# Performance work log

Measured on AMD Instinct MI355X. Metric: run time of the kernel, lower is better.

Reference implementation:

```python
import jax, jax.numpy as jnp
import numpy as np

N = 500_000      # number of gaussians
F = 32           # grid feature dim (WavePlaneField.feat_dim)
R = 128          # plane resolution
W = 256          # MLP width
BOUNDS = 1.6     # scene aabb half-extent (args.bounds)


def setup_inputs() -> dict:
    key = jax.random.key(0)
    ks = jax.random.split(key, 16)
    s = lambda d: 1.0 / np.sqrt(d)
    return {
        "rays_pts_emb": jax.random.normal(ks[0], (N, 3), jnp.float32),
        "rotations_emb": jax.random.normal(ks[1], (N, 4), jnp.float32),
        "scale_emb": jax.random.uniform(ks[2], (N, 3), jnp.float32),
        "shs_emb": jax.random.normal(ks[3], (N, 16, 3), jnp.float32),
        "view_dir": jax.random.normal(ks[4], (N, 3), jnp.float32),
        "time_emb": jax.random.uniform(ks[5], (N, 1), jnp.float32),
        "h_emb": jax.random.normal(ks[6], (N, 2), jnp.float32),
        # multiplicative k-planes: init near 1 so products are well-scaled
        "space_planes": 1.0 + 0.1 * jax.random.normal(ks[7], (3, R, R, F), jnp.float32),
        "time_planes": 1.0 + 0.1 * jax.random.normal(ks[8], (3, R, R, F), jnp.float32),
        "w_enc": s(F) * jax.random.normal(ks[9], (F, W), jnp.float32),
        "b_enc": jnp.zeros((W,), jnp.float32),
        "w1": s(W) * jax.random.normal(ks[10], (W, W), jnp.float32),
        "b1": jnp.zeros((W,), jnp.float32),
        "w2": s(W) * jax.random.normal(ks[11], (W, 16 * 3), jnp.float32),
        "b2": jnp.zeros((16 * 3,), jnp.float32),
    }


def _interp2d(plane, u, v):
    """Bilinear sample plane [R,R,F] at normalized coords u,v in [0,1]. -> [N,F]"""
    Rr = plane.shape[0]
    x = jnp.clip(u, 0.0, 1.0) * (Rr - 1)
    y = jnp.clip(v, 0.0, 1.0) * (Rr - 1)
    x0 = jnp.clip(jnp.floor(x), 0, Rr - 2).astype(jnp.int32)
    y0 = jnp.clip(jnp.floor(y), 0, Rr - 2).astype(jnp.int32)
    fx = (x - x0)[:, None]
    fy = (y - y0)[:, None]
    p00 = plane[y0, x0]
    p01 = plane[y0, x0 + 1]
    p10 = plane[y0 + 1, x0]
    p11 = plane[y0 + 1, x0 + 1]
    return (p00 * (1 - fx) + p01 * fx) * (1 - fy) + (p10 * (1 - fx) + p11 * fx) * fy


def _covariance(scale, rotation):
    """3DGS: L = R(q) @ diag(s); cov = L L^T; return 6 unique entries [N,6]."""
    q = rotation / jnp.linalg.norm(rotation, axis=-1, keepdims=True)
    r, x, y, z = q[:, 0], q[:, 1], q[:, 2], q[:, 3]
    Rm = jnp.stack([
        jnp.stack([1 - 2 * (y * y + z * z), 2 * (x * y - r * z), 2 * (x * z + r * y)], -1),
        jnp.stack([2 * (x * y + r * z), 1 - 2 * (x * x + z * z), 2 * (y * z - r * x)], -1),
        jnp.stack([2 * (x * z - r * y), 2 * (y * z + r * x), 1 - 2 * (x * x + y * y)], -1),
    ], axis=1)  # [N,3,3]
    L = Rm * scale[:, None, :]                      # R @ diag(s)
    cov = jnp.einsum('nij,nkj->nik', L, L)          # L @ L^T
    return jnp.stack([cov[:, 0, 0], cov[:, 0, 1], cov[:, 0, 2],
                      cov[:, 1, 1], cov[:, 1, 2], cov[:, 2, 2]], axis=-1)


def reference(rays_pts_emb, rotations_emb, scale_emb, shs_emb, view_dir, time_emb,
              h_emb, space_planes, time_planes, w_enc, b_enc, w1, b1, w2, b2):
    # quaternion -> covariance (passed into grid in original; grid lookup itself
    # only needs positions/time, so symm is computed but unused downstream)
    symm = _covariance(scale_emb, rotations_emb)

    pts = rays_pts_emb[:, :3]
    pn = jnp.clip(pts / BOUNDS, -1.0, 1.0) * 0.5 + 0.5  # aabb-normalize to [0,1]
    xn, yn, zn = pn[:, 0], pn[:, 1], pn[:, 2]
    t = jnp.clip(time_emb[:, 0], 0.0, 1.0)

    space = (_interp2d(space_planes[0], xn, yn)
             * _interp2d(space_planes[1], xn, zn)
             * _interp2d(space_planes[2], yn, zn))          # [N,F]
    spacetime = (_interp2d(time_planes[0], xn, t)
                 * _interp2d(time_planes[1], yn, t)
                 * _interp2d(time_planes[2], zn, t))        # [N,F]

    feat = (space * spacetime) @ w_enc + b_enc              # spacetime_enc (Linear only)
    h = jax.nn.relu(feat) @ w1 + b1                         # shs_deform MLP
    d = jax.nn.relu(h) @ w2 + b2                            # [N,48]
    shs = shs_emb + d.reshape(-1, 16, 3)

    del symm  # original forward discards covariance after grid query
    return (rays_pts_emb, rotations_emb, h_emb[:, 0:1], shs)
```

## Files before the change

kernel.cpp:

```cpp
#include <hip/hip_runtime.h>
#include <hip/hip_fp16.h>

#define NPTS 500000
#define RPLANE 128
#define FDIM 32
#define PLSZ (RPLANE * RPLANE * FDIM)

typedef __bf16 bfx8 __attribute__((ext_vector_type(8)));
typedef float f32x4 __attribute__((ext_vector_type(4)));

__device__ __forceinline__ unsigned short f2bf(float f) {
    unsigned int u = __builtin_bit_cast(unsigned int, f);
    unsigned int r = (u + 0x7FFFu + ((u >> 16) & 1u)) >> 16;
    return (unsigned short)r;
}

__device__ __forceinline__ bfx8 ld_frag_g(const unsigned short* p) {
    uint4 raw = *(const uint4*)p;
    return __builtin_bit_cast(bfx8, raw);
}

struct h4v { __half2 a, b; };

__device__ __forceinline__ float4 interp4h(const __half* __restrict__ plane,
                                           float u, float v, int f0) {
    float x = fminf(fmaxf(u, 0.f), 1.f) * 127.0f;
    float y = fminf(fmaxf(v, 0.f), 1.f) * 127.0f;
    float xf = fminf(fmaxf(floorf(x), 0.f), 126.f);
    float yf = fminf(fmaxf(floorf(y), 0.f), 126.f);
    int x0 = (int)xf, y0 = (int)yf;
    float fx = x - xf, fy = y - yf;
    const __half* p = plane + (size_t)(y0 * RPLANE + x0) * FDIM + f0;
    h4v c00 = *(const h4v*)p;
    h4v c01 = *(const h4v*)(p + FDIM);
    h4v c10 = *(const h4v*)(p + RPLANE * FDIM);
    h4v c11 = *(const h4v*)(p + RPLANE * FDIM + FDIM);
    float2 a00l = __half22float2(c00.a), a00h = __half22float2(c00.b);
    float2 a01l = __half22float2(c01.a), a01h = __half22float2(c01.b);
    float2 a10l = __half22float2(c10.a), a10h = __half22float2(c10.b);
    float2 a11l = __half22float2(c11.a), a11h = __half22float2(c11.b);
    float w00 = (1.f - fx) * (1.f - fy);
    float w01 = fx * (1.f - fy);
    float w10 = (1.f - fx) * fy;
    float w11 = fx * fy;
    float4 r;
    r.x = a00l.x * w00 + a01l.x * w01 + a10l.x * w10 + a11l.x * w11;
    r.y = a00l.y * w00 + a01l.y * w01 + a10l.y * w10 + a11l.y * w11;
    r.z = a00h.x * w00 + a01h.x * w01 + a10h.x * w10 + a11h.x * w11;
    r.w = a00h.y * w00 + a01h.y * w01 + a10h.y * w10 + a11h.y * w11;
    return r;
}

__global__ void prep_all(const float* __restrict__ wenc, const float* __restrict__ w1,
                         const float* __restrict__ w2, const float* __restrict__ spf,
                         const float* __restrict__ tpf,
                         unsigned short* __restrict__ wf, __half* __restrict__ ph) {
    const int WTOT = 86016;
    const int PTOT = 6 * PLSZ;
    const int total = WTOT + PTOT;
    for (int i = blockIdx.x * blockDim.x + threadIdx.x; i < total;
         i += gridDim.x * blockDim.x) {
        if (i < WTOT) {
            const float* W;
            unsigned short* dst;
            int K, Ncols, idx;
            if (i < 8192)       { W = wenc; K = 32;  Ncols = 256; idx = i;         dst = wf; }
            else if (i < 73728) { W = w1;   K = 256; Ncols = 256; idx = i - 8192;  dst = wf + 8192; }
            else                { W = w2;   K = 256; Ncols = 48;  idx = i - 73728; dst = wf + 73728; }
            int j = idx & 7;
            int l = (idx >> 3) & 63;
            int b = idx >> 9;
            int KS = K >> 5;
            int ct = b / KS;
            int ks = b - ct * KS;
            int k = ks * 32 + ((l >> 4) << 3) + j;
            int col = ct * 16 + (l & 15);
            dst[idx] = f2bf(W[(size_t)k * Ncols + col]);
        } else {
            int j = i - WTOT;
            float v = (j < 3 * PLSZ) ? spf[j] : tpf[j - 3 * PLSZ];
            ph[j] = __float2half(v);
        }
    }
}

__global__ void pass_copy(const float* __restrict__ rays, const float* __restrict__ rot,
                          const float* __restrict__ h, float* __restrict__ out) {
    const int total = NPTS * 8;
    for (int i = blockIdx.x * blockDim.x + threadIdx.x; i < total; i += gridDim.x * blockDim.x) {
        float v;
        if (i < NPTS * 3) v = rays[i];
        else if (i < NPTS * 7) v = rot[i - NPTS * 3];
        else v = h[(i - NPTS * 7) * 2];
        out[i] = v;
    }
}

__global__ __launch_bounds__(256, 2) void fused2(
    const float* __restrict__ rays, const float* __restrict__ tme,
    const float* __restrict__ shs,
    const __half* __restrict__ sp, const __half* __restrict__ tp,
    const unsigned short* __restrict__ wf,
    const float* __restrict__ benc, const float* __restrict__ b1v,
    const float* __restrict__ b2v, float* __restrict__ out) {
    __shared__ unsigned short feat[4][32][40];
    __shared__ unsigned short hbuf[4][32][264];
    const int tid = threadIdx.x;
    const int wid = tid >> 6;
    const int lane = tid & 63;
    const int p0 = blockIdx.x * 128 + wid * 32;
    if (p0 >= NPTS) return;
    unsigned short(*fw)[40] = feat[wid];
    unsigned short(*hw)[264] = hbuf[wid];

#pragma unroll
    for (int it = 0; it < 4; ++it) {
        int task = it * 64 + lane;
        int pl = task >> 3;
        int fg = task & 7;
        int p = p0 + pl;
        float4 g = make_float4(0.f, 0.f, 0.f, 0.f);
        if (p < NPTS) {
            float px = rays[p * 3 + 0], py = rays[p * 3 + 1], pz = rays[p * 3 + 2];
            const float inv = 0.625f;
            float xn = fminf(fmaxf(px * inv, -1.f), 1.f) * 0.5f + 0.5f;
            float yn = fminf(fmaxf(py * inv, -1.f), 1.f) * 0.5f + 0.5f;
            float zn = fminf(fmaxf(pz * inv, -1.f), 1.f) * 0.5f + 0.5f;
            float t = fminf(fmaxf(tme[p], 0.f), 1.f);
            int f0 = fg << 2;
            float4 s0 = interp4h(sp, xn, yn, f0);
            float4 s1 = interp4h(sp + PLSZ, xn, zn, f0);
            float4 s2 = interp4h(sp + 2 * PLSZ, yn, zn, f0);
            float4 t0 = interp4h(tp, xn, t, f0);
            float4 t1 = interp4h(tp + PLSZ, yn, t, f0);
            float4 t2 = interp4h(tp + 2 * PLSZ, zn, t, f0);
            g.x = s0.x * s1.x * s2.x * t0.x * t1.x * t2.x;
            g.y = s0.y * s1.y * s2.y * t0.y * t1.y * t2.y;
            g.z = s0.z * s1.z * s2.z * t0.z * t1.z * t2.z;
            g.w = s0.w * s1.w * s2.w * t0.w * t1.w * t2.w;
        }
        ushort4 gb;
        gb.x = f2bf(g.x); gb.y = f2bf(g.y); gb.z = f2bf(g.z); gb.w = f2bf(g.w);
        *(ushort4*)&fw[pl][fg << 2] = gb;
    }

    const int lrow = lane & 15;
    const int lk8 = (lane >> 4) << 3;
    const int drow = (lane >> 4) << 2;

    bfx8 a0 = __builtin_bit_cast(bfx8, *(const uint4*)&fw[lrow][lk8]);
    bfx8 a1 = __builtin_bit_cast(bfx8, *(const uint4*)&fw[16 + lrow][lk8]);
#pragma unroll
    for (int ct = 0; ct < 16; ++ct) {
        bfx8 b = ld_frag_g(wf + (size_t)ct * 512 + lane * 8);
        f32x4 z = {0.f, 0.f, 0.f, 0.f};
        f32x4 d0 = __builtin_amdgcn_mfma_f32_16x16x32_bf16(a0, b, z, 0, 0, 0);
        f32x4 d1 = __builtin_amdgcn_mfma_f32_16x16x32_bf16(a1, b, z, 0, 0, 0);
        float bias = benc[ct * 16 + lrow];
#pragma unroll
        for (int r = 0; r < 4; ++r) {
            hw[drow + r][ct * 16 + lrow] = f2bf(fmaxf(d0[r] + bias, 0.f));
            hw[16 + drow + r][ct * 16 + lrow] = f2bf(fmaxf(d1[r] + bias, 0.f));
        }
    }

    const unsigned short* w1f = wf + 8192;
    bfx8 A0[8], A1[8];
#pragma unroll
    for (int ks = 0; ks < 8; ++ks) {
        A0[ks] = __builtin_bit_cast(bfx8, *(const uint4*)&hw[lrow][ks * 32 + lk8]);
        A1[ks] = __builtin_bit_cast(bfx8, *(const uint4*)&hw[16 + lrow][ks * 32 + lk8]);
    }
#pragma unroll
    for (int ct = 0; ct < 16; ++ct) {
        f32x4 acc0 = {0.f, 0.f, 0.f, 0.f};
        f32x4 acc1 = {0.f, 0.f, 0.f, 0.f};
#pragma unroll
        for (int ks = 0; ks < 8; ++ks) {
            bfx8 B = ld_frag_g(w1f + (size_t)(ct * 8 + ks) * 512 + lane * 8);
            acc0 = __builtin_amdgcn_mfma_f32_16x16x32_bf16(A0[ks], B, acc0, 0, 0, 0);
            acc1 = __builtin_amdgcn_mfma_f32_16x16x32_bf16(A1[ks], B, acc1, 0, 0, 0);
        }
        float bias = b1v[ct * 16 + lrow];
#pragma unroll
        for (int r = 0; r < 4; ++r) {
            hw[drow + r][ct * 16 + lrow] = f2bf(fmaxf(acc0[r] + bias, 0.f));
            hw[16 + drow + r][ct * 16 + lrow] = f2bf(fmaxf(acc1[r] + bias, 0.f));
        }
    }

    const unsigned short* w2f = wf + 73728;
    bfx8 C0[8], C1[8];
#pragma unroll
    for (int ks = 0; ks < 8; ++ks) {
        C0[ks] = __builtin_bit_cast(bfx8, *(const uint4*)&hw[lrow][ks * 32 + lk8]);
        C1[ks] = __builtin_bit_cast(bfx8, *(const uint4*)&hw[16 + lrow][ks * 32 + lk8]);
    }
#pragma unroll
    for (int ct = 0; ct < 3; ++ct) {
        f32x4 acc0 = {0.f, 0.f, 0.f, 0.f};
        f32x4 acc1 = {0.f, 0.f, 0.f, 0.f};
#pragma unroll
        for (int ks = 0; ks < 8; ++ks) {
            bfx8 B = ld_frag_g(w2f + (size_t)(ct * 8 + ks) * 512 + lane * 8);
            acc0 = __builtin_amdgcn_mfma_f32_16x16x32_bf16(C0[ks], B, acc0, 0, 0, 0);
            acc1 = __builtin_amdgcn_mfma_f32_16x16x32_bf16(C1[ks], B, acc1, 0, 0, 0);
        }
        int col = ct * 16 + lrow;
        float bias = b2v[col];
#pragma unroll
        for (int r = 0; r < 4; ++r) {
            int pr = p0 + drow + r;
            if (pr < NPTS)
                out[(size_t)NPTS * 8 + (size_t)pr * 48 + col] =
                    shs[(size_t)pr * 48 + col] + acc0[r] + bias;
            int pr2 = p0 + 16 + drow + r;
            if (pr2 < NPTS)
                out[(size_t)NPTS * 8 + (size_t)pr2 * 48 + col] =
                    shs[(size_t)pr2 * 48 + col] + acc1[r] + bias;
        }
    }
}

extern "C" void kernel_launch(void* const* d_in, const int* in_sizes, int n_in,
                              void* d_out, int out_size, void* d_ws, size_t ws_size,
                              hipStream_t stream) {
    const float* rays = (const float*)d_in[0];
    const float* rot  = (const float*)d_in[1];
    const float* shs  = (const float*)d_in[3];
    const float* tme  = (const float*)d_in[5];
    const float* h_e  = (const float*)d_in[6];
    const float* spf  = (const float*)d_in[7];
    const float* tpf  = (const float*)d_in[8];
    const float* wenc = (const float*)d_in[9];
    const float* benc = (const float*)d_in[10];
    const float* w1   = (const float*)d_in[11];
    const float* b1v  = (const float*)d_in[12];
    const float* w2   = (const float*)d_in[13];
    const float* b2v  = (const float*)d_in[14];
    float* out = (float*)d_out;
    unsigned short* wf = (unsigned short*)d_ws;
    __half* ph = (__half*)(wf + 86016);

    prep_all<<<3408, 256, 0, stream>>>(wenc, w1, w2, spf, tpf, wf, ph);
    pass_copy<<<2048, 256, 0, stream>>>(rays, rot, h_e, out);
    fused2<<<(NPTS + 127) / 128, 256, 0, stream>>>(
        rays, tme, shs, ph, ph + 3 * PLSZ, wf, benc, b1v, b2v, out);
}
```

Before: 239.1 us.

## Shrink per-wave tile to 16 points, compute features in MFMA layout with half2 math

Each wave now handles 16 points instead of 32, and the fused kernel's launch bounds allow 4 blocks per CU, so occupancy should rise. Each lane computes 8 features for one point directly in the MFMA A-fragment layout. That removes the feature staging buffer in shared memory and uses 16-byte plane loads. Bilinear interpolation and the product of the six planes are done in packed fp16 arithmetic, which cuts ALU work but lowers precision. The hidden activations are stored in a smaller XOR-swizzled shared buffer to avoid bank conflicts, at the cost of reloading the weight fragments for only half as many points per load.

```diff
diff --git a/kernel.cpp b/kernel.cpp
--- a/kernel.cpp
+++ b/kernel.cpp
@@ -9,6 +9,8 @@
 typedef __bf16 bfx8 __attribute__((ext_vector_type(8)));
 typedef float f32x4 __attribute__((ext_vector_type(4)));
 
+struct U8 { unsigned short s[8]; };
+
 __device__ __forceinline__ unsigned short f2bf(float f) {
     unsigned int u = __builtin_bit_cast(unsigned int, f);
     unsigned int r = (u + 0x7FFFu + ((u >> 16) & 1u)) >> 16;
@@ -20,35 +22,8 @@
     return __builtin_bit_cast(bfx8, raw);
 }
 
-struct h4v { __half2 a, b; };
-
-__device__ __forceinline__ float4 interp4h(const __half* __restrict__ plane,
-                                           float u, float v, int f0) {
-    float x = fminf(fmaxf(u, 0.f), 1.f) * 127.0f;
-    float y = fminf(fmaxf(v, 0.f), 1.f) * 127.0f;
-    float xf = fminf(fmaxf(floorf(x), 0.f), 126.f);
-    float yf = fminf(fmaxf(floorf(y), 0.f), 126.f);
-    int x0 = (int)xf, y0 = (int)yf;
-    float fx = x - xf, fy = y - yf;
-    const __half* p = plane + (size_t)(y0 * RPLANE + x0) * FDIM + f0;
-    h4v c00 = *(const h4v*)p;
-    h4v c01 = *(const h4v*)(p + FDIM);
-    h4v c10 = *(const h4v*)(p + RPLANE * FDIM);
-    h4v c11 = *(const h4v*)(p + RPLANE * FDIM + FDIM);
-    float2 a00l = __half22float2(c00.a), a00h = __half22float2(c00.b);
-    float2 a01l = __half22float2(c01.a), a01h = __half22float2(c01.b);
-    float2 a10l = __half22float2(c10.a), a10h = __half22float2(c10.b);
-    float2 a11l = __half22float2(c11.a), a11h = __half22float2(c11.b);
-    float w00 = (1.f - fx) * (1.f - fy);
-    float w01 = fx * (1.f - fy);
-    float w10 = (1.f - fx) * fy;
-    float w11 = fx * fy;
-    float4 r;
-    r.x = a00l.x * w00 + a01l.x * w01 + a10l.x * w10 + a11l.x * w11;
-    r.y = a00l.y * w00 + a01l.y * w01 + a10l.y * w10 + a11l.y * w11;
-    r.z = a00h.x * w00 + a01h.x * w01 + a10h.x * w10 + a11h.x * w11;
-    r.w = a00h.y * w00 + a01h.y * w01 + a10h.y * w10 + a11h.y * w11;
-    return r;
+__device__ __forceinline__ __half2 u2h(unsigned u) {
+    return __builtin_bit_cast(__half2, u);
 }
 
 __global__ void prep_all(const float* __restrict__ wenc, const float* __restrict__ w1,
@@ -96,128 +71,142 @@
     }
 }
 
-__global__ __launch_bounds__(256, 2) void fused2(
+__global__ __launch_bounds__(256, 4) void fused3(
     const float* __restrict__ rays, const float* __restrict__ tme,
-    const float* __restrict__ shs,
-    const __half* __restrict__ sp, const __half* __restrict__ tp,
+    const float* __restrict__ shs, const __half* __restrict__ ph,
     const unsigned short* __restrict__ wf,
     const float* __restrict__ benc, const float* __restrict__ b1v,
     const float* __restrict__ b2v, float* __restrict__ out) {
-    __shared__ unsigned short feat[4][32][40];
-    __shared__ unsigned short hbuf[4][32][264];
+    __shared__ unsigned short hbuf[4][16 * 256];
     const int tid = threadIdx.x;
     const int wid = tid >> 6;
     const int lane = tid & 63;
-    const int p0 = blockIdx.x * 128 + wid * 32;
+    const int p0 = blockIdx.x * 64 + wid * 16;
     if (p0 >= NPTS) return;
-    unsigned short(*fw)[40] = feat[wid];
-    unsigned short(*hw)[264] = hbuf[wid];
-
-#pragma unroll
-    for (int it = 0; it < 4; ++it) {
-        int task = it * 64 + lane;
-        int pl = task >> 3;
-        int fg = task & 7;
-        int p = p0 + pl;
-        float4 g = make_float4(0.f, 0.f, 0.f, 0.f);
-        if (p < NPTS) {
-            float px = rays[p * 3 + 0], py = rays[p * 3 + 1], pz = rays[p * 3 + 2];
-            const float inv = 0.625f;
-            float xn = fminf(fmaxf(px * inv, -1.f), 1.f) * 0.5f + 0.5f;
-            float yn = fminf(fmaxf(py * inv, -1.f), 1.f) * 0.5f + 0.5f;
-            float zn = fminf(fmaxf(pz * inv, -1.f), 1.f) * 0.5f + 0.5f;
-            float t = fminf(fmaxf(tme[p], 0.f), 1.f);
-            int f0 = fg << 2;
-            float4 s0 = interp4h(sp, xn, yn, f0);
-            float4 s1 = interp4h(sp + PLSZ, xn, zn, f0);
-            float4 s2 = interp4h(sp + 2 * PLSZ, yn, zn, f0);
-            float4 t0 = interp4h(tp, xn, t, f0);
-            float4 t1 = interp4h(tp + PLSZ, yn, t, f0);
-            float4 t2 = interp4h(tp + 2 * PLSZ, zn, t, f0);
-            g.x = s0.x * s1.x * s2.x * t0.x * t1.x * t2.x;
-            g.y = s0.y * s1.y * s2.y * t0.y * t1.y * t2.y;
-            g.z = s0.z * s1.z * s2.z * t0.z * t1.z * t2.z;
-            g.w = s0.w * s1.w * s2.w * t0.w * t1.w * t2.w;
-        }
-        ushort4 gb;
-        gb.x = f2bf(g.x); gb.y = f2bf(g.y); gb.z = f2bf(g.z); gb.w = f2bf(g.w);
-        *(ushort4*)&fw[pl][fg << 2] = gb;
-    }
+    char* hw = (char*)hbuf[wid];
 
     const int lrow = lane & 15;
-    const int lk8 = (lane >> 4) << 3;
-    const int drow = (lane >> 4) << 2;
-
-    bfx8 a0 = __builtin_bit_cast(bfx8, *(const uint4*)&fw[lrow][lk8]);
-    bfx8 a1 = __builtin_bit_cast(bfx8, *(const uint4*)&fw[16 + lrow][lk8]);
+    const int lg = lane >> 4;
+    const int drow = lg << 2;
+    const int pt = p0 + lrow;
+    const int f0 = lg << 3;
+
+    float px = rays[pt * 3 + 0], py = rays[pt * 3 + 1], pz = rays[pt * 3 + 2];
+    const float inv = 0.625f;
+    float xn = fminf(fmaxf(px * inv, -1.f), 1.f) * 0.5f + 0.5f;
+    float yn = fminf(fmaxf(py * inv, -1.f), 1.f) * 0.5f + 0.5f;
+    float zn = fminf(fmaxf(pz * inv, -1.f), 1.f) * 0.5f + 0.5f;
+    float tt = fminf(fmaxf(tme[pt], 0.f), 1.f);
+
+    float c4[4] = {xn, yn, zn, tt};
+    int i0[4];
+    float fr[4];
+#pragma unroll
+    for (int c = 0; c < 4; ++c) {
+        float x = c4[c] * 127.0f;
+        float xf = fminf(floorf(x), 126.0f);
+        i0[c] = (int)xf;
+        fr[c] = x - xf;
+    }
+    const int uc[6] = {0, 0, 1, 0, 1, 2};
+    const int vc[6] = {1, 2, 2, 3, 3, 3};
+
+    __half2 g2[4];
+#pragma unroll
+    for (int pl = 0; pl < 6; ++pl) {
+        int x0 = i0[uc[pl]], y0 = i0[vc[pl]];
+        float fx = fr[uc[pl]], fy = fr[vc[pl]];
+        const __half* base = ph + (size_t)pl * PLSZ + ((y0 * RPLANE + x0) << 5) + f0;
+        uint4 q00 = *(const uint4*)base;
+        uint4 q01 = *(const uint4*)(base + FDIM);
+        uint4 q10 = *(const uint4*)(base + RPLANE * FDIM);
+        uint4 q11 = *(const uint4*)(base + RPLANE * FDIM + FDIM);
+        __half2 wa = __float2half2_rn((1.f - fx) * (1.f - fy));
+        __half2 wb = __float2half2_rn(fx * (1.f - fy));
+        __half2 wc = __float2half2_rn((1.f - fx) * fy);
+        __half2 wd = __float2half2_rn(fx * fy);
+        unsigned qa[4] = {q00.x, q00.y, q00.z, q00.w};
+        unsigned qb[4] = {q01.x, q01.y, q01.z, q01.w};
+        unsigned qc[4] = {q10.x, q10.y, q10.z, q10.w};
+        unsigned qd[4] = {q11.x, q11.y, q11.z, q11.w};
+#pragma unroll
+        for (int i = 0; i < 4; ++i) {
+            __half2 r = __hmul2(u2h(qa[i]), wa);
+            r = __hfma2(u2h(qb[i]), wb, r);
+            r = __hfma2(u2h(qc[i]), wc, r);
+            r = __hfma2(u2h(qd[i]), wd, r);
+            g2[i] = (pl == 0) ? r : __hmul2(g2[i], r);
+        }
+    }
+    U8 af;
+#pragma unroll
+    for (int i = 0; i < 4; ++i) {
+        float2 v = __half22float2(g2[i]);
+        af.s[2 * i] = f2bf(v.x);
+        af.s[2 * i + 1] = f2bf(v.y);
+    }
+    bfx8 a1 = __builtin_bit_cast(bfx8, af);
+
 #pragma unroll
     for (int ct = 0; ct < 16; ++ct) {
         bfx8 b = ld_frag_g(wf + (size_t)ct * 512 + lane * 8);
         f32x4 z = {0.f, 0.f, 0.f, 0.f};
-        f32x4 d0 = __builtin_amdgcn_mfma_f32_16x16x32_bf16(a0, b, z, 0, 0, 0);
-        f32x4 d1 = __builtin_amdgcn_mfma_f32_16x16x32_bf16(a1, b, z, 0, 0, 0);
+        f32x4 d = __builtin_amdgcn_mfma_f32_16x16x32_bf16(a1, b, z, 0, 0, 0);
         float bias = benc[ct * 16 + lrow];
 #pragma unroll
         for (int r = 0; r < 4; ++r) {
-            hw[drow + r][ct * 16 + lrow] = f2bf(fmaxf(d0[r] + bias, 0.f));
-            hw[16 + drow + r][ct * 16 + lrow] = f2bf(fmaxf(d1[r] + bias, 0.f));
+            int row = drow + r;
+            int off = ((row << 9) + (ct << 5) + (lrow << 1)) ^ ((row & 7) << 4);
+            *(unsigned short*)(hw + off) = f2bf(fmaxf(d[r] + bias, 0.f));
         }
     }
 
     const unsigned short* w1f = wf + 8192;
-    bfx8 A0[8], A1[8];
+    bfx8 A2[8];
 #pragma unroll
     for (int ks = 0; ks < 8; ++ks) {
-        A0[ks] = __builtin_bit_cast(bfx8, *(const uint4*)&hw[lrow][ks * 32 + lk8]);
-        A1[ks] = __builtin_bit_cast(bfx8, *(const uint4*)&hw[16 + lrow][ks * 32 + lk8]);
+        int off = ((lrow << 9) + (ks << 6) + (lg << 4)) ^ ((lrow & 7) << 4);
+        A2[ks] = __builtin_bit_cast(bfx8, *(uint4*)(hw + off));
     }
 #pragma unroll
     for (int ct = 0; ct < 16; ++ct) {
-        f32x4 acc0 = {0.f, 0.f, 0.f, 0.f};
-        f32x4 acc1 = {0.f, 0.f, 0.f, 0.f};
+        f32x4 acc = {0.f, 0.f, 0.f, 0.f};
 #pragma unroll
         for (int ks = 0; ks < 8; ++ks) {
             bfx8 B = ld_frag_g(w1f + (size_t)(ct * 8 + ks) * 512 + lane * 8);
-            acc0 = __builtin_amdgcn_mfma_f32_16x16x32_bf16(A0[ks], B, acc0, 0, 0, 0);
-            acc1 = __builtin_amdgcn_mfma_f32_16x16x32_bf16(A1[ks], B, acc1, 0, 0, 0);
+            acc = __builtin_amdgcn_mfma_f32_16x16x32_bf16(A2[ks], B, acc, 0, 0, 0);
         }
         float bias = b1v[ct * 16 + lrow];
 #pragma unroll
         for (int r = 0; r < 4; ++r) {
-            hw[drow + r][ct * 16 + lrow] = f2bf(fmaxf(acc0[r] + bias, 0.f));
-            hw[16 + drow + r][ct * 16 + lrow] = f2bf(fmaxf(acc1[r] + bias, 0.f));
+            int row = drow + r;
+            int off = ((row << 9) + (ct << 5) + (lrow << 1)) ^ ((row & 7) << 4);
+            *(unsigned short*)(hw + off) = f2bf(fmaxf(acc[r] + bias, 0.f));
         }
     }
 
     const unsigned short* w2f = wf + 73728;
-    bfx8 C0[8], C1[8];
+    bfx8 A3[8];
 #pragma unroll
     for (int ks = 0; ks < 8; ++ks) {
-        C0[ks] = __builtin_bit_cast(bfx8, *(const uint4*)&hw[lrow][ks * 32 + lk8]);
-        C1[ks] = __builtin_bit_cast(bfx8, *(const uint4*)&hw[16 + lrow][ks * 32 + lk8]);
+        int off = ((lrow << 9) + (ks << 6) + (lg << 4)) ^ ((lrow & 7) << 4);
+        A3[ks] = __builtin_bit_cast(bfx8, *(uint4*)(hw + off));
     }
 #pragma unroll
     for (int ct = 0; ct < 3; ++ct) {
-        f32x4 acc0 = {0.f, 0.f, 0.f, 0.f};
-        f32x4 acc1 = {0.f, 0.f, 0.f, 0.f};
+        f32x4 acc = {0.f, 0.f, 0.f, 0.f};
 #pragma unroll
         for (int ks = 0; ks < 8; ++ks) {
             bfx8 B = ld_frag_g(w2f + (size_t)(ct * 8 + ks) * 512 + lane * 8);
-            acc0 = __builtin_amdgcn_mfma_f32_16x16x32_bf16(C0[ks], B, acc0, 0, 0, 0);
-            acc1 = __builtin_amdgcn_mfma_f32_16x16x32_bf16(C1[ks], B, acc1, 0, 0, 0);
+            acc = __builtin_amdgcn_mfma_f32_16x16x32_bf16(A3[ks], B, acc, 0, 0, 0);
         }
         int col = ct * 16 + lrow;
         float bias = b2v[col];
 #pragma unroll
         for (int r = 0; r < 4; ++r) {
             int pr = p0 + drow + r;
-            if (pr < NPTS)
-                out[(size_t)NPTS * 8 + (size_t)pr * 48 + col] =
-                    shs[(size_t)pr * 48 + col] + acc0[r] + bias;
-            int pr2 = p0 + 16 + drow + r;
-            if (pr2 < NPTS)
-                out[(size_t)NPTS * 8 + (size_t)pr2 * 48 + col] =
-                    shs[(size_t)pr2 * 48 + col] + acc1[r] + bias;
+            out[(size_t)NPTS * 8 + (size_t)pr * 48 + col] =
+                shs[(size_t)pr * 48 + col] + acc[r] + bias;
         }
     }
 }
@@ -244,6 +233,6 @@
 
     prep_all<<<3408, 256, 0, stream>>>(wenc, w1, w2, spf, tpf, wf, ph);
     pass_copy<<<2048, 256, 0, stream>>>(rays, rot, h_e, out);
-    fused2<<<(NPTS + 127) / 128, 256, 0, stream>>>(
-        rays, tme, shs, ph, ph + 3 * PLSZ, wf, benc, b1v, b2v, out);
-}
+    fused3<<<(NPTS + 63) / 64, 256, 0, stream>>>(
+        rays, tme, shs, ph, wf, benc, b1v, b2v, out);
+}
```

After: 418.5 us. 1.75x slower.
